# Kernel tuning notes

Measured on AMD Instinct MI355X. Metric: run time of the kernel, lower is better.

## Reference

```python
import jax, jax.numpy as jnp
import numpy as np

FACTOR = 1.0
KERNEL = 3
PAD = 1
STRIDE = 1


def setup_inputs() -> dict:
    key = jax.random.key(0)
    ks = jax.random.split(key, 7)
    B_, Cin, Cout, L, CODE = 32, 128, 128, 4096, 2
    return {
        "input": jax.random.normal(ks[0], (B_, Cin, L), dtype=jnp.float32),
        "codes": jax.random.normal(ks[1], (B_, CODE, CODE), dtype=jnp.float32),
        "weight": jax.random.normal(ks[2], (Cout, Cin, KERNEL), dtype=jnp.float32) * 0.05,
        "A": jax.random.normal(ks[3], (Cin, CODE, KERNEL), dtype=jnp.float32) * 0.05,
        "B": jax.random.normal(ks[4], (Cout, CODE, KERNEL), dtype=jnp.float32) * 0.05,
        "bias": jax.random.normal(ks[5], (Cout,), dtype=jnp.float32) * 0.05,
        "bias_context": jax.random.normal(ks[6], (CODE, Cout), dtype=jnp.float32) * 0.05,
    }


def reference(input, codes, weight, A, B, bias, bias_context):
    # Hypernetwork-generated per-sample conv weights (low-rank via codes)
    w = jnp.einsum('ick,bcr->birk', A, codes)            # (b, in, code, k)
    context_w = jnp.einsum('birk,ork->boik', w, B)       # (b, out, in, k)
    combined_weight = weight + FACTOR * context_w        # (b, out, in, k)

    diag = jnp.diagonal(codes, axis1=-2, axis2=-1)       # (b, code)
    context_bias = diag @ bias_context                   # (b, out)
    combined_bias = bias + FACTOR * context_bias         # (b, out)

    # circular padding along spatial axis
    padded = jnp.pad(input, ((0, 0), (0, 0), (PAD, PAD)), mode='wrap')
    L_out = (input.shape[-1] + 2 * PAD - KERNEL) // STRIDE + 1
    # windowed view: (b, in, L_out, k) via k shifted slices (k is tiny, loop ok)
    windows = jnp.stack([padded[:, :, j:j + L_out * STRIDE:STRIDE] for j in range(KERNEL)], axis=-1)
    out = jnp.einsum('bihw,boiw->boh', windows, combined_weight)
    return out + combined_bias[..., None]
```

## Files before the change

### kernel.cpp

```cpp
#include <hip/hip_runtime.h>
#include <hip/hip_bf16.h>
#include <stdint.h>
#include <stddef.h>

#define L_LEN 4096
#define CIN   128
#define COUT  128
#define NB    32
#define KTOT  384
#define TN    128
#define ROWS  (TN + 2)

typedef __bf16 bf16x8 __attribute__((ext_vector_type(8)));
typedef float  f32x4  __attribute__((ext_vector_type(4)));

__device__ __forceinline__ uint16_t f2bf(float f) {
    union { float f; uint32_t u; } v; v.f = f;
    return (uint16_t)((v.u + 0x7fffu + ((v.u >> 16) & 1u)) >> 16);
}
__device__ __forceinline__ uint32_t pack2(float lo, float hi) {
    return (uint32_t)f2bf(lo) | ((uint32_t)f2bf(hi) << 16);
}

__global__ __launch_bounds__(256) void geps_combine(
    const float* __restrict__ codes, const float* __restrict__ weight,
    const float* __restrict__ Amat,  const float* __restrict__ Bmat,
    const float* __restrict__ bias,  const float* __restrict__ bias_ctx,
    uint16_t* __restrict__ Wc, float* __restrict__ cbias)
{
    int tid = blockIdx.x * 256 + threadIdx.x;
    if (tid < NB * COUT * KTOT) {
        int b   = tid / (COUT * KTOT);
        int rem = tid % (COUT * KTOT);
        int o   = rem / KTOT;
        int kp  = rem % KTOT;
        int k   = kp >> 7;
        int i   = kp & 127;
        float cw = 0.f;
        #pragma unroll
        for (int c = 0; c < 2; ++c) {
            float a = Amat[i * 6 + c * 3 + k];
            #pragma unroll
            for (int r = 0; r < 2; ++r)
                cw += a * codes[b * 4 + c * 2 + r] * Bmat[o * 6 + r * 3 + k];
        }
        float val = weight[o * 384 + i * 3 + k] + cw;
        Wc[tid] = f2bf(val);
    }
    if (tid < NB * COUT) {
        int b = tid >> 7, o = tid & 127;
        float cb = bias[o];
        #pragma unroll
        for (int c = 0; c < 2; ++c)
            cb += codes[b * 4 + c * 2 + c] * bias_ctx[c * 128 + o];
        cbias[tid] = cb;
    }
}

__global__ __launch_bounds__(256, 2) void geps_conv(
    const float* __restrict__ in, const uint16_t* __restrict__ Wc,
    const float* __restrict__ cbias, float* __restrict__ out)
{
    __shared__ uint16_t __attribute__((aligned(16))) Xt[ROWS * 128];
    __shared__ float cb[COUT];

    const int tid  = threadIdx.x;
    const int b    = blockIdx.y;
    const int h0   = blockIdx.x * TN;
    const int lane = tid & 63;
    const int wid  = tid >> 6;
    const int m16  = lane & 15;
    const int q    = lane >> 4;
    const int mq   = wid * 32;

    if (tid < COUT) cb[tid] = cbias[b * COUT + tid];

    const uint16_t* WcB = Wc + (size_t)b * COUT * KTOT;
    const float*    inb = in + (size_t)b * CIN * L_LEN;

    bf16x8 af[12][2];
    #pragma unroll
    for (int t = 0; t < 12; ++t)
        #pragma unroll
        for (int mt = 0; mt < 2; ++mt)
            af[t][mt] = *(const bf16x8*)(WcB +
                (size_t)(mq + mt * 16 + m16) * KTOT + t * 32 + q * 8);

    #pragma unroll
    for (int it = 0; it < 4; ++it) {
        int task = it * 256 + tid;
        int p4   = task >> 5;
        int qd   = task & 31;
        const float* r0 = inb + (size_t)(4 * p4) * L_LEN + h0 + 4 * qd;
        float4 a0 = *(const float4*)(r0);
        float4 a1 = *(const float4*)(r0 + L_LEN);
        float4 a2 = *(const float4*)(r0 + 2 * L_LEN);
        float4 a3 = *(const float4*)(r0 + 3 * L_LEN);
        const int off = (4 * p4) & 7;
        const int pc  = p4 >> 1;
        const float v0[4] = {a0.x, a0.y, a0.z, a0.w};
        const float v1[4] = {a1.x, a1.y, a1.z, a1.w};
        const float v2[4] = {a2.x, a2.y, a2.z, a2.w};
        const float v3[4] = {a3.x, a3.y, a3.z, a3.w};
        #pragma unroll
        for (int j = 0; j < 4; ++j) {
            int r  = 1 + 4 * qd + j;
            int ch = pc ^ (r & 15);
            uint2 w;
            w.x = pack2(v0[j], v1[j]);
            w.y = pack2(v2[j], v3[j]);
            *(uint2*)&Xt[r * 128 + (ch << 3) + off] = w;
        }
    }
    if (tid < 128) {
        int p    = tid & 63;
        int side = tid >> 6;
        int r    = side ? (ROWS - 1) : 0;
        int gh   = (h0 - 1 + r) & (L_LEN - 1);
        float x0 = inb[(size_t)(2 * p)     * L_LEN + gh];
        float x1 = inb[(size_t)(2 * p + 1) * L_LEN + gh];
        int chunk = (p >> 2) ^ (r & 15);
        *(uint32_t*)&Xt[r * 128 + (chunk << 3) + ((2 * p) & 7)] = pack2(x0, x1);
    }

    f32x4 acc[2][8];
    #pragma unroll
    for (int a = 0; a < 2; ++a)
        #pragma unroll
        for (int c = 0; c < 8; ++c) acc[a][c] = 0.0f;

    __syncthreads();

    #pragma unroll
    for (int t = 0; t < 12; ++t) {
        const int k   = t >> 2;
        const int i0c = (t & 3) * 4;
        bf16x8 bf[8];
        #pragma unroll
        for (int nt = 0; nt < 8; ++nt) {
            int r  = nt * 16 + m16 + k;
            int ch = (i0c + q) ^ (r & 15);
            bf[nt] = *(const bf16x8*)&Xt[r * 128 + (ch << 3)];
        }
        #pragma unroll
        for (int mt = 0; mt < 2; ++mt)
            #pragma unroll
            for (int nt = 0; nt < 8; ++nt)
                acc[mt][nt] = __builtin_amdgcn_mfma_f32_16x16x32_bf16(
                    af[t][mt], bf[nt], acc[mt][nt], 0, 0, 0);
    }

    float* outb = out + (size_t)b * COUT * L_LEN + h0;
    #pragma unroll
    for (int mt = 0; mt < 2; ++mt) {
        #pragma unroll
        for (int reg = 0; reg < 4; ++reg) {
            int o = mq + mt * 16 + q * 4 + reg;
            float bv = cb[o];
            float* orow = outb + (size_t)o * L_LEN;
            #pragma unroll
            for (int nt = 0; nt < 8; ++nt) {
                int h = nt * 16 + m16;
                orow[h] = acc[mt][nt][reg] + bv;
            }
        }
    }
}

extern "C" void kernel_launch(void* const* d_in, const int* in_sizes, int n_in,
                              void* d_out, int out_size, void* d_ws, size_t ws_size,
                              hipStream_t stream) {
    const float* input    = (const float*)d_in[0];
    const float* codes    = (const float*)d_in[1];
    const float* weight   = (const float*)d_in[2];
    const float* Amat     = (const float*)d_in[3];
    const float* Bmat     = (const float*)d_in[4];
    const float* bias     = (const float*)d_in[5];
    const float* bias_ctx = (const float*)d_in[6];
    float* out = (float*)d_out;

    uint16_t* Wc    = (uint16_t*)d_ws;
    float*    cbias = (float*)((char*)d_ws + (size_t)NB * COUT * KTOT * 2);

    geps_combine<<<dim3((NB * COUT * KTOT) / 256), 256, 0, stream>>>(
        codes, weight, Amat, Bmat, bias, bias_ctx, Wc, cbias);
    geps_conv<<<dim3(L_LEN / TN, NB), 256, 0, stream>>>(input, Wc, cbias, out);
}
```

Before: 139.9 us.

## Halve conv tile, pre-swizzle weights for coalesced per-wave streaming loads

The combine kernel now writes the per-sample weights in the exact per-wave MFMA fragment order, so each wave loads its A-operand with contiguous 16-byte lane loads. The conv kernel streams these fragments one K-step at a time, prefetching the next step, instead of holding all 24 fragments in registers. The spatial tile drops from 128 to 64 and launch bounds ask for 4 blocks per SM, giving more blocks and higher occupancy. Output stores become nontemporal. The trade-off is that weights are reloaded twice as often (once per smaller tile) and the non-unrolled loop adds load latency on each step.

Result: no change. 138.5 us (-1.0%).

```diff
diff --git a/kernel.cpp b/kernel.cpp
--- a/kernel.cpp
+++ b/kernel.cpp
@@ -8,7 +8,7 @@
 #define COUT  128
 #define NB    32
 #define KTOT  384
-#define TN    128
+#define TN    64
 #define ROWS  (TN + 2)
 
 typedef __bf16 bf16x8 __attribute__((ext_vector_type(8)));
@@ -30,12 +30,18 @@
 {
     int tid = blockIdx.x * 256 + threadIdx.x;
     if (tid < NB * COUT * KTOT) {
-        int b   = tid / (COUT * KTOT);
-        int rem = tid % (COUT * KTOT);
-        int o   = rem / KTOT;
-        int kp  = rem % KTOT;
-        int k   = kp >> 7;
-        int i   = kp & 127;
+        int j    = tid & 7;
+        int lane = (tid >> 3) & 63;
+        int mt   = (tid >> 9) & 1;
+        int tmp  = tid >> 10;
+        int t    = tmp % 12;
+        int bo   = tmp / 12;
+        int og   = bo & 3;
+        int b    = bo >> 2;
+        int col  = t * 32 + (lane >> 4) * 8 + j;
+        int k    = col >> 7;
+        int i    = col & 127;
+        int o    = og * 32 + mt * 16 + (lane & 15);
         float cw = 0.f;
         #pragma unroll
         for (int c = 0; c < 2; ++c) {
@@ -57,7 +63,7 @@
     }
 }
 
-__global__ __launch_bounds__(256, 2) void geps_conv(
+__global__ __launch_bounds__(256, 4) void geps_conv(
     const float* __restrict__ in, const uint16_t* __restrict__ Wc,
     const float* __restrict__ cbias, float* __restrict__ out)
 {
@@ -75,22 +81,17 @@
 
     if (tid < COUT) cb[tid] = cbias[b * COUT + tid];
 
-    const uint16_t* WcB = Wc + (size_t)b * COUT * KTOT;
-    const float*    inb = in + (size_t)b * CIN * L_LEN;
+    const float* inb = in + (size_t)b * CIN * L_LEN;
 
-    bf16x8 af[12][2];
-    #pragma unroll
-    for (int t = 0; t < 12; ++t)
-        #pragma unroll
-        for (int mt = 0; mt < 2; ++mt)
-            af[t][mt] = *(const bf16x8*)(WcB +
-                (size_t)(mq + mt * 16 + m16) * KTOT + t * 32 + q * 8);
+    const uint16_t* WcW = Wc + (size_t)(b * 4 + wid) * 12288 + lane * 8;
+    bf16x8 ac0 = *(const bf16x8*)(WcW);
+    bf16x8 ac1 = *(const bf16x8*)(WcW + 512);
 
     #pragma unroll
-    for (int it = 0; it < 4; ++it) {
+    for (int it = 0; it < 2; ++it) {
         int task = it * 256 + tid;
-        int p4   = task >> 5;
-        int qd   = task & 31;
+        int p4   = task >> 4;
+        int qd   = task & 15;
         const float* r0 = inb + (size_t)(4 * p4) * L_LEN + h0 + 4 * qd;
         float4 a0 = *(const float4*)(r0);
         float4 a1 = *(const float4*)(r0 + L_LEN);
@@ -123,31 +124,35 @@
         *(uint32_t*)&Xt[r * 128 + (chunk << 3) + ((2 * p) & 7)] = pack2(x0, x1);
     }
 
-    f32x4 acc[2][8];
+    f32x4 acc[2][4];
     #pragma unroll
     for (int a = 0; a < 2; ++a)
         #pragma unroll
-        for (int c = 0; c < 8; ++c) acc[a][c] = 0.0f;
+        for (int c = 0; c < 4; ++c) acc[a][c] = 0.0f;
 
     __syncthreads();
 
-    #pragma unroll
+    #pragma unroll 1
     for (int t = 0; t < 12; ++t) {
+        const uint16_t* pn = WcW + ((t + 1 < 12) ? (t + 1) : 11) * 1024;
+        bf16x8 an0 = *(const bf16x8*)(pn);
+        bf16x8 an1 = *(const bf16x8*)(pn + 512);
+
         const int k   = t >> 2;
-        const int i0c = (t & 3) * 4;
-        bf16x8 bf[8];
+        const int i0c = (t & 3) << 2;
+        bf16x8 bf[4];
         #pragma unroll
-        for (int nt = 0; nt < 8; ++nt) {
+        for (int nt = 0; nt < 4; ++nt) {
             int r  = nt * 16 + m16 + k;
             int ch = (i0c + q) ^ (r & 15);
             bf[nt] = *(const bf16x8*)&Xt[r * 128 + (ch << 3)];
         }
         #pragma unroll
-        for (int mt = 0; mt < 2; ++mt)
-            #pragma unroll
-            for (int nt = 0; nt < 8; ++nt)
-                acc[mt][nt] = __builtin_amdgcn_mfma_f32_16x16x32_bf16(
-                    af[t][mt], bf[nt], acc[mt][nt], 0, 0, 0);
+        for (int nt = 0; nt < 4; ++nt) {
+            acc[0][nt] = __builtin_amdgcn_mfma_f32_16x16x32_bf16(ac0, bf[nt], acc[0][nt], 0, 0, 0);
+            acc[1][nt] = __builtin_amdgcn_mfma_f32_16x16x32_bf16(ac1, bf[nt], acc[1][nt], 0, 0, 0);
+        }
+        ac0 = an0; ac1 = an1;
     }
 
     float* outb = out + (size_t)b * COUT * L_LEN + h0;
@@ -159,10 +164,9 @@
             float bv = cb[o];
             float* orow = outb + (size_t)o * L_LEN;
             #pragma unroll
-            for (int nt = 0; nt < 8; ++nt) {
-                int h = nt * 16 + m16;
-                orow[h] = acc[mt][nt][reg] + bv;
-            }
+            for (int nt = 0; nt < 4; ++nt)
+                __builtin_nontemporal_store(acc[mt][nt][reg] + bv,
+                                            &orow[nt * 16 + m16]);
         }
     }
 }
```
